# Kernel tuning notes

Hardware: AMD Instinct MI355X
Metric: run time of the kernel (lower is better)

The kernel has to match this reference:

```python
import jax, jax.numpy as jnp
import numpy as np

RADIUS = 1.0
NSAMPLE = 8
GROUPS = 8
EPS = 1e-5


def setup_inputs() -> dict:
    key = jax.random.key(0)
    ks = jax.random.split(key, 8)
    b, n_p, dim, C = 4, 4096, 128, 64
    coords = jax.random.normal(ks[0], (b, n_p, 3), jnp.float32)
    xyz2 = jax.random.normal(ks[1], (b, n_p, 3), jnp.float32)
    fmap1 = jax.random.normal(ks[2], (b, dim, n_p), jnp.float32)
    fmap2 = jax.random.normal(ks[3], (b, dim, n_p), jnp.float32)
    conv_w = jax.random.normal(ks[4], (C, 4), jnp.float32) * 0.1
    conv_b = jnp.zeros((C,), jnp.float32)
    gn_gamma = jnp.ones((C,), jnp.float32)
    gn_beta = jnp.zeros((C,), jnp.float32)
    prelu_a = jnp.full((1,), 0.25, jnp.float32)
    out_w = jax.random.normal(ks[5], (C, C), jnp.float32) * 0.1
    out_b = jnp.zeros((C,), jnp.float32)
    return {"coords": coords, "xyz2": xyz2, "fmap1": fmap1, "fmap2": fmap2,
            "conv_w": conv_w, "conv_b": conv_b, "gn_gamma": gn_gamma,
            "gn_beta": gn_beta, "prelu_a": prelu_a, "out_w": out_w, "out_b": out_b}


def ball_query(xyz2, coords, radius, nsample):
    # first-nsample points of xyz2 within `radius` of each query in coords,
    # padded with the first valid index (0 if none) -- matches PointNet++ ball query.
    n = xyz2.shape[1]
    d2 = jnp.sum((coords[:, :, None, :] - xyz2[:, None, :, :]) ** 2, axis=-1)  # [b,m,n]
    j = jnp.arange(n, dtype=jnp.float32)
    score = jnp.where(d2 < radius * radius, -j, -float(n))  # larger score = earlier valid idx
    vals, _ = jax.lax.top_k(score, nsample)  # [b,m,nsample]
    valid = vals > -float(n)
    idx = (-vals).astype(jnp.int32)
    first = jnp.where(valid[..., :1], idx[..., :1], 0)
    return jnp.where(valid, idx, first)  # [b,m,nsample]


def reference(coords, xyz2, fmap1, fmap2, conv_w, conv_b, gn_gamma, gn_beta, prelu_a, out_w, out_b):
    b, n_p, _ = coords.shape
    dim = fmap1.shape[1]
    # corr = fmap1^T fmap2 / sqrt(dim): [b, n_p, n_p]
    corr = jnp.einsum('bdn,bdm->bnm', fmap1, fmap2) / jnp.sqrt(jnp.float32(dim))
    idx = ball_query(xyz2, coords, RADIUS, NSAMPLE)  # [b,n_p,nsample]
    # grouped_xyz: xyz2[idx] - coords -> [b, 3, n_p, nsample]
    gathered = jax.vmap(lambda pts, ind: pts[ind])(xyz2, idx)  # [b,n_p,ns,3]
    grouped_xyz = jnp.transpose(gathered - coords[:, :, None, :], (0, 3, 1, 2))
    # corr gather along source dim
    cur_corr = jnp.take_along_axis(corr, idx, axis=2)[:, None]  # [b,1,n_p,ns]
    feat = jnp.concatenate([cur_corr, grouped_xyz], axis=1)  # [b,4,n_p,ns]
    # 1x1 Conv2d
    x = jnp.einsum('oc,bcns->bons', conv_w, feat) + conv_b[None, :, None, None]
    # GroupNorm(8, 64)
    C = x.shape[1]
    xg = x.reshape(b, GROUPS, C // GROUPS, n_p, NSAMPLE)
    mu = jnp.mean(xg, axis=(2, 3, 4), keepdims=True)
    var = jnp.var(xg, axis=(2, 3, 4), keepdims=True)
    xg = (xg - mu) * jax.lax.rsqrt(var + EPS)
    x = xg.reshape(b, C, n_p, NSAMPLE) * gn_gamma[None, :, None, None] + gn_beta[None, :, None, None]
    # PReLU (single shared slope)
    x = jnp.where(x >= 0, x, prelu_a[0] * x)
    # max over neighbors
    x = jnp.max(x, axis=3)  # [b,64,n_p]
    # 1x1 Conv1d out
    return jnp.einsum('oc,bcn->bon', out_w, x) + out_b[None, :, None]
```

## Files before the change

### kernel.cpp

```cpp
#include <hip/hip_runtime.h>
#include <hip/hip_cooperative_groups.h>
#include <math.h>

namespace cg = cooperative_groups;

#define B 4
#define NP 4096
#define DIM 128
#define CCH 64
#define NS 8

struct TrS { float tile[128][31]; };
struct K2S { float As[16 * 132]; float red[4][14]; };
struct K3S {
  float4 vs4[256]; float4 ow4[1024];
  float cw[256], cb[64], Av[64], Bv[64], ob[64];
  float red2[8][14], Sm[14], SxA[64], SxxA[64];
};
struct SM {
  float4 fs4[128];
  int sidx[128];
  union { TrS tr; K2S k2; K3S k3; } u;
};

__global__ __launch_bounds__(256, 4) void fused_all(
    const float* __restrict__ coords, const float* __restrict__ xyz2,
    const float* __restrict__ f1, const float* __restrict__ f2,
    const float* __restrict__ conv_w, const float* __restrict__ conv_b,
    const float* __restrict__ gamma, const float* __restrict__ beta,
    const float* __restrict__ prelu, const float* __restrict__ out_w,
    const float* __restrict__ out_b, float* __restrict__ out,
    float* __restrict__ f2T, float* __restrict__ parts, int useT) {
  cg::grid_group grid = cg::this_grid();
  __shared__ SM sm;
  int blk = blockIdx.x;
  int t = threadIdx.x;
  int bq = (blk & 7) >> 1;
  int chunk = ((blk >> 3) << 1) | (blk & 1);
  int m0 = chunk * 16;

  if (useT) {
    int b = blk >> 8;
    int n0 = (blk & 255) * 16;
    const float* s = f2 + (size_t)b * DIM * NP;
    float* dd = f2T + (size_t)b * NP * DIM;
#pragma unroll
    for (int it = 0; it < 2; ++it) {
      int f = t + it * 256;
      int d = f >> 2, ng = f & 3;
      float4 v = *(const float4*)&s[(size_t)d * NP + n0 + ng * 4];
      int aw = 5 * (d >> 5);
      sm.u.tr.tile[d][ng * 4 + 0 + aw] = v.x;
      sm.u.tr.tile[d][ng * 4 + 1 + aw] = v.y;
      sm.u.tr.tile[d][ng * 4 + 2 + aw] = v.z;
      sm.u.tr.tile[d][ng * 4 + 3 + aw] = v.w;
    }
    __syncthreads();
#pragma unroll
    for (int it = 0; it < 2; ++it) {
      int f = t + it * 256;
      int n = f >> 5, dg = f & 31;
      int ar = 5 * (dg >> 3);
      float4 w;
      w.x = sm.u.tr.tile[dg * 4 + 0][n + ar];
      w.y = sm.u.tr.tile[dg * 4 + 1][n + ar];
      w.z = sm.u.tr.tile[dg * 4 + 2][n + ar];
      w.w = sm.u.tr.tile[dg * 4 + 3][n + ar];
      *(float4*)&dd[(size_t)(n0 + n) * DIM + dg * 4] = w;
    }
  }

  {
    int wv = t >> 6, lane = t & 63;
    const float* xz = xyz2 + (size_t)bq * NP * 3;
#pragma unroll 1
    for (int qi = 0; qi < 4; ++qi) {
      int m = m0 + wv * 4 + qi;
      const float* cp = coords + ((size_t)bq * NP + m) * 3;
      float cx = cp[0], cy = cp[1], cz = cp[2];
      int j0 = lane * 3;
      float px = xz[j0], py = xz[j0 + 1], pz = xz[j0 + 2];
      int cnt = 0, first = 0;
      bool any = false;
      for (int c = 0; c < 64 && cnt < NS; ++c) {
        int cn = (c < 63) ? c + 1 : 63;
        int jn = (cn * 64 + lane) * 3;
        float nx = xz[jn], ny = xz[jn + 1], nz = xz[jn + 2];
        float dx = __fsub_rn(cx, px);
        float dy = __fsub_rn(cy, py);
        float dz = __fsub_rn(cz, pz);
        float d2 = __fadd_rn(__fadd_rn(__fmul_rn(dx, dx), __fmul_rn(dy, dy)),
                             __fmul_rn(dz, dz));
        bool hit = d2 < 1.0f;
        unsigned long long mk = __ballot(hit);
        if (mk) {
          int rank = cnt + __popcll(mk & ((1ull << lane) - 1ull));
          if (hit && rank < NS) sm.sidx[(wv * 4 + qi) * NS + rank] = c * 64 + lane;
          if (!any) {
            first = c * 64 + (__ffsll((long long)mk) - 1);
            any = true;
          }
          cnt += __popcll(mk);
        }
        px = nx; py = ny; pz = nz;
      }
      if (lane < NS && lane >= cnt)
        sm.sidx[(wv * 4 + qi) * NS + lane] = first;
    }
  }

  grid.sync();

  {
    K2S& k2 = sm.u.k2;
    int b = bq;
    if (useT) {
#pragma unroll
      for (int pass = 0; pass < 2; ++pass) {
        int d = pass * 64 + (t >> 2);
        int j4 = t & 3;
        float4 v = *(const float4*)&f1[(size_t)(b * DIM + d) * NP + m0 + j4 * 4];
        k2.As[(j4 * 4 + 0) * 132 + d] = v.x;
        k2.As[(j4 * 4 + 1) * 132 + d] = v.y;
        k2.As[(j4 * 4 + 2) * 132 + d] = v.z;
        k2.As[(j4 * 4 + 3) * 132 + d] = v.w;
      }
    }
    __syncthreads();

    int g = t >> 3;
    int l = t & 7;
    int idv[4];
#pragma unroll
    for (int r = 0; r < 4; ++r) idv[r] = sm.sidx[r * 32 + g];

    float pm[14];
#pragma unroll
    for (int k = 0; k < 14; ++k) pm[k] = 0.f;

#pragma unroll
    for (int r = 0; r < 4; ++r) {
      int pi = r * 32 + g;
      int m = pi >> 3;
      int id = idv[r];
      float acc = 0.f;
      if (useT) {
        const float4* brow = (const float4*)(f2T + ((size_t)b * NP + id) * DIM);
        const float4* arow = (const float4*)&k2.As[m * 132];
#pragma unroll
        for (int k = 0; k < 4; ++k) {
          float4 y = brow[l + 8 * k];
          float4 x = arow[l + 8 * k];
          acc += x.x * y.x + x.y * y.y + x.z * y.z + x.w * y.w;
        }
      } else {
#pragma unroll
        for (int k = 0; k < 4; ++k) {
#pragma unroll
          for (int c = 0; c < 4; ++c) {
            int d = (l + 8 * k) * 4 + c;
            acc += f1[(size_t)(b * DIM + d) * NP + m0 + m] *
                   f2[(size_t)(b * DIM + d) * NP + id];
          }
        }
      }
      acc += __shfl_xor(acc, 1);
      acc += __shfl_xor(acc, 2);
      acc += __shfl_xor(acc, 4);
      float corr = acc * 0.08838834764831843f;
      const float* cp = coords + ((size_t)b * NP + m0 + m) * 3;
      const float* xp = xyz2 + ((size_t)b * NP + id) * 3;
      float dx = xp[0] - cp[0], dy = xp[1] - cp[1], dz = xp[2] - cp[2];
      if (l == 0) {
        float4 fv;
        fv.x = corr; fv.y = dx; fv.z = dy; fv.w = dz;
        sm.fs4[pi] = fv;
      }
      pm[0] += corr; pm[1] += dx; pm[2] += dy; pm[3] += dz;
      pm[4] += corr * corr; pm[5] += corr * dx; pm[6] += corr * dy;
      pm[7] += corr * dz; pm[8] += dx * dx; pm[9] += dx * dy;
      pm[10] += dx * dz; pm[11] += dy * dy; pm[12] += dy * dz; pm[13] += dz * dz;
    }
#pragma unroll
    for (int k = 0; k < 14; ++k) {
      float v = pm[k];
#pragma unroll
      for (int off = 32; off; off >>= 1) v += __shfl_xor(v, off);
      pm[k] = v;
    }
    int lane = t & 63, wvv = t >> 6;
    if (lane == 0) {
#pragma unroll
      for (int k = 0; k < 14; ++k) k2.red[wvv][k] = pm[k];
    }
    __syncthreads();
    if (t < 14) {
      float ssum = (k2.red[0][t] + k2.red[1][t] + k2.red[2][t] + k2.red[3][t]) * 0.125f;
      parts[((size_t)bq * 256 + chunk) * 14 + t] = ssum;
    }
  }

  grid.sync();

  {
    K3S& kb = sm.u.k3;
    int b = bq;
    int n0 = m0;
    {
      const float4* src = (const float4*)out_w;
#pragma unroll
      for (int k = 0; k < 4; ++k) {
        int i4 = t + k * 256;
        int oo = i4 >> 4, gg = i4 & 15;
        kb.ow4[oo * 16 + (gg ^ ((oo >> 2) & 7))] = src[i4];
      }
    }
    kb.cw[t] = conv_w[t];
    if (t < 64) {
      kb.cb[t] = conv_b[t];
      kb.ob[t] = out_b[t];
    }
    if (t < 112) {
      int k = t % 14, jg = t / 14;
      float s = 0.f;
      const float* pp = parts + ((size_t)b * 256 + jg * 32) * 14 + k;
      for (int j = 0; j < 32; ++j) s += pp[j * 14];
      kb.red2[jg][k] = s;
    }
    float alpha = prelu[0];
    __syncthreads();
    if (t < 14) {
      float s = 0.f;
#pragma unroll
      for (int jg = 0; jg < 8; ++jg) s += kb.red2[jg][t];
      kb.Sm[t] = s;
    }
    __syncthreads();
    if (t < 64) {
      int o = t;
      float w0 = kb.cw[o * 4 + 0], w1 = kb.cw[o * 4 + 1];
      float w2 = kb.cw[o * 4 + 2], w3 = kb.cw[o * 4 + 3];
      float bo = kb.cb[o];
      const float cnt = (float)(NP * NS);
      float wS1 = w0 * kb.Sm[0] + w1 * kb.Sm[1] + w2 * kb.Sm[2] + w3 * kb.Sm[3];
      float q = w0 * w0 * kb.Sm[4] + w1 * w1 * kb.Sm[8] + w2 * w2 * kb.Sm[11] +
                w3 * w3 * kb.Sm[13] +
                2.f * (w0 * w1 * kb.Sm[5] + w0 * w2 * kb.Sm[6] + w0 * w3 * kb.Sm[7] +
                       w1 * w2 * kb.Sm[9] + w1 * w3 * kb.Sm[10] + w2 * w3 * kb.Sm[12]);
      kb.SxA[o] = wS1 + bo * cnt;
      kb.SxxA[o] = q + 2.f * bo * wS1 + bo * bo * cnt;
    }
    __syncthreads();
    if (t < 64) {
      int o = t, g = o >> 3;
      const float cnt = (float)(NP * NS);
      float sm_ = 0.f, s2 = 0.f;
#pragma unroll
      for (int k = 0; k < 8; ++k) {
        sm_ += kb.SxA[g * 8 + k];
        s2 += kb.SxxA[g * 8 + k];
      }
      float mean = sm_ / (cnt * 8.f);
      float e2 = s2 / (cnt * 8.f);
      float var = e2 - mean * mean;
      float inv = rsqrtf(var + 1e-5f);
      float A = gamma[o] * inv;
      kb.Av[o] = A;
      kb.Bv[o] = beta[o] - mean * A;
    }
    __syncthreads();

    {
      int o = t & 63;
      int pw = t >> 6;
      float w0 = kb.cw[o * 4 + 0], w1 = kb.cw[o * 4 + 1];
      float w2 = kb.cw[o * 4 + 2], w3 = kb.cw[o * 4 + 3];
      float A = kb.Av[o], Bc = kb.Bv[o], bb = kb.cb[o];
      float* vsf = (float*)kb.vs4;
#pragma unroll
      for (int i = 0; i < 4; ++i) {
        int p = pw * 4 + i;
        float mx = -INFINITY;
#pragma unroll
        for (int s = 0; s < NS; ++s) {
          float4 f = sm.fs4[p * 8 + s];
          float x = fmaf(w0, f.x, fmaf(w1, f.y, fmaf(w2, f.z, fmaf(w3, f.w, bb))));
          float y = fmaf(A, x, Bc);
          y = (y >= 0.f) ? y : alpha * y;
          mx = fmaxf(mx, y);
        }
        vsf[(p * 16 + ((o >> 2) ^ ((p >> 2) & 7))) * 4 + (o & 3)] = mx;
      }
    }
    __syncthreads();

    {
      int ti = t >> 3;
      int tj = t & 7;
      float acc[2][2];
#pragma unroll
      for (int oi = 0; oi < 2; ++oi)
#pragma unroll
        for (int pj = 0; pj < 2; ++pj) acc[oi][pj] = 0.f;
#pragma unroll
      for (int g = 0; g < 16; ++g) {
        float4 vv[2], ww[2];
#pragma unroll
        for (int pj = 0; pj < 2; ++pj) {
          int p = tj * 2 + pj;
          vv[pj] = kb.vs4[p * 16 + (g ^ ((p >> 2) & 7))];
        }
#pragma unroll
        for (int oi = 0; oi < 2; ++oi) {
          int oo = ti * 2 + oi;
          ww[oi] = kb.ow4[oo * 16 + (g ^ ((oo >> 2) & 7))];
        }
#pragma unroll
        for (int oi = 0; oi < 2; ++oi)
#pragma unroll
          for (int pj = 0; pj < 2; ++pj) {
            acc[oi][pj] = fmaf(ww[oi].x, vv[pj].x, acc[oi][pj]);
            acc[oi][pj] = fmaf(ww[oi].y, vv[pj].y, acc[oi][pj]);
            acc[oi][pj] = fmaf(ww[oi].z, vv[pj].z, acc[oi][pj]);
            acc[oi][pj] = fmaf(ww[oi].w, vv[pj].w, acc[oi][pj]);
          }
      }
#pragma unroll
      for (int oi = 0; oi < 2; ++oi) {
        int oo = ti * 2 + oi;
        float bb = kb.ob[oo];
        float2 r;
        r.x = acc[oi][0] + bb;
        r.y = acc[oi][1] + bb;
        *(float2*)&out[((size_t)b * CCH + oo) * NP + n0 + tj * 2] = r;
      }
    }
  }
}

__global__ __launch_bounds__(256) void kA_bq_transpose(
    const float* __restrict__ coords, const float* __restrict__ xyz2,
    int* __restrict__ idxb, const float* __restrict__ f2,
    float* __restrict__ o2) {
  int blk = blockIdx.x;
  int t = threadIdx.x;
  __shared__ float tile[128][33];
  if (blk < B * NP) {
    int b = blk >> 12, m = blk & (NP - 1);
    int wv = t >> 6, lane = t & 63;
    const float* cp = coords + ((size_t)b * NP + m) * 3;
    float cx = cp[0], cy = cp[1], cz = cp[2];
    const float* xz = xyz2 + (size_t)b * NP * 3;
    int base = wv * 1024;
    int j0 = (base + lane) * 3;
    float px = xz[j0], py = xz[j0 + 1], pz = xz[j0 + 2];
    int cnt = 0, myidx = 0;
    for (int c = 0; c < 16 && cnt < NS; ++c) {
      int cn = (c < 15) ? c + 1 : 15;
      int jn = (base + cn * 64 + lane) * 3;
      float nx = xz[jn], ny = xz[jn + 1], nz = xz[jn + 2];
      float dx = __fsub_rn(cx, px);
      float dy = __fsub_rn(cy, py);
      float dz = __fsub_rn(cz, pz);
      float d2 = __fadd_rn(__fadd_rn(__fmul_rn(dx, dx), __fmul_rn(dy, dy)),
                           __fmul_rn(dz, dz));
      unsigned long long mk = __ballot(d2 < 1.0f);
      while (mk && cnt < NS) {
        int bpos = __ffsll(mk) - 1;
        int jf = base + c * 64 + bpos;
        if (lane == cnt) myidx = jf;
        ++cnt;
        mk &= mk - 1;
      }
      px = nx; py = ny; pz = nz;
    }
    __shared__ int sidx[4][NS];
    __shared__ int scnt[4];
    if (lane < NS) sidx[wv][lane] = myidx;
    if (lane == 0) scnt[wv] = cnt;
    __syncthreads();
    if (t < NS) {
      int c0 = scnt[0], c1 = scnt[1], c2 = scnt[2], c3 = scnt[3];
      int total = c0 + c1 + c2 + c3;
      int v;
      if (t < c0) v = sidx[0][t];
      else if (t < c0 + c1) v = sidx[1][t - c0];
      else if (t < c0 + c1 + c2) v = sidx[2][t - c0 - c1];
      else if (t < total) v = sidx[3][t - c0 - c1 - c2];
      else v = (c0 > 0) ? sidx[0][0]
             : (c1 > 0) ? sidx[1][0]
             : (c2 > 0) ? sidx[2][0]
             : (c3 > 0) ? sidx[3][0] : 0;
      idxb[((size_t)b * NP + m) * NS + t] = v;
    }
  } else {
    int tb = blk - B * NP;
    int b = tb >> 7;
    int n0 = (tb & 127) * 32;
    const float* s = f2 + (size_t)b * DIM * NP;
    float* d = o2 + (size_t)b * NP * DIM;
    int dr = t >> 3;
    int ng = t & 7;
#pragma unroll
    for (int k = 0; k < 4; ++k) {
      int dd = dr + 32 * k;
      float4 v = *(const float4*)&s[(size_t)dd * NP + n0 + ng * 4];
      tile[dd][ng * 4 + 0] = v.x;
      tile[dd][ng * 4 + 1] = v.y;
      tile[dd][ng * 4 + 2] = v.z;
      tile[dd][ng * 4 + 3] = v.w;
    }
    __syncthreads();
    int n = t >> 3;
#pragma unroll
    for (int k = 0; k < 4; ++k) {
      int d0 = (t & 7) * 4 + 32 * k;
      float4 w;
      w.x = tile[d0 + 0][n];
      w.y = tile[d0 + 1][n];
      w.z = tile[d0 + 2][n];
      w.w = tile[d0 + 3][n];
      *(float4*)&d[(size_t)(n0 + n) * DIM + d0] = w;
    }
  }
}

__global__ __launch_bounds__(256) void k2_corrfeat(
    const float* __restrict__ f1, const float* __restrict__ f2T,
    const float* __restrict__ coords, const float* __restrict__ xyz2,
    const int* __restrict__ idxb, float* __restrict__ feat,
    float* __restrict__ parts, int trans) {
  int i = blockIdx.x;
  int b = (i & 7) >> 1;
  int chunk = ((i >> 3) << 1) | (i & 1);
  int m0 = chunk * 16;
  int t = threadIdx.x;
  __shared__ float As[16 * 132];
  __shared__ float red[4][14];
  if (trans) {
#pragma unroll
    for (int pass = 0; pass < 2; ++pass) {
      int d = pass * 64 + (t >> 2);
      int j4 = t & 3;
      float4 v = *(const float4*)&f1[(size_t)(b * DIM + d) * NP + m0 + j4 * 4];
      As[(j4 * 4 + 0) * 132 + d] = v.x;
      As[(j4 * 4 + 1) * 132 + d] = v.y;
      As[(j4 * 4 + 2) * 132 + d] = v.z;
      As[(j4 * 4 + 3) * 132 + d] = v.w;
    }
  }
  __syncthreads();
  int g = t >> 3;
  int l = t & 7;
  size_t ibase = ((size_t)b * NP + m0) * NS;
  int idv[4];
#pragma unroll
  for (int r = 0; r < 4; ++r) idv[r] = idxb[ibase + r * 32 + g];
  float pm[14];
#pragma unroll
  for (int k = 0; k < 14; ++k) pm[k] = 0.f;
#pragma unroll
  for (int r = 0; r < 4; ++r) {
    int pi = r * 32 + g;
    int m = pi >> 3, s = pi & 7;
    int id = idv[r];
    float acc = 0.f;
    if (trans) {
      const float4* brow = (const float4*)(f2T + ((size_t)b * NP + id) * DIM);
      const float4* arow = (const float4*)&As[m * 132];
#pragma unroll
      for (int k = 0; k < 4; ++k) {
        float4 y = brow[l + 8 * k];
        float4 x = arow[l + 8 * k];
        acc += x.x * y.x + x.y * y.y + x.z * y.z + x.w * y.w;
      }
    } else {
#pragma unroll
      for (int k = 0; k < 4; ++k) {
#pragma unroll
        for (int c = 0; c < 4; ++c) {
          int d = (l + 8 * k) * 4 + c;
          acc += f1[(size_t)(b * DIM + d) * NP + m0 + m] *
                 f2T[(size_t)(b * DIM + d) * NP + id];
        }
      }
    }
    acc += __shfl_xor(acc, 1);
    acc += __shfl_xor(acc, 2);
    acc += __shfl_xor(acc, 4);
    float corr = acc * 0.08838834764831843f;
    const float* cp = coords + ((size_t)b * NP + m0 + m) * 3;
    const float* xp = xyz2 + ((size_t)b * NP + id) * 3;
    float dx = xp[0] - cp[0], dy = xp[1] - cp[1], dz = xp[2] - cp[2];
    if (l == 0) {
      float4 fv;
      fv.x = corr; fv.y = dx; fv.z = dy; fv.w = dz;
      ((float4*)feat)[((size_t)b * NP + m0 + m) * NS + s] = fv;
    }
    pm[0] += corr; pm[1] += dx; pm[2] += dy; pm[3] += dz;
    pm[4] += corr * corr; pm[5] += corr * dx; pm[6] += corr * dy;
    pm[7] += corr * dz; pm[8] += dx * dx; pm[9] += dx * dy;
    pm[10] += dx * dz; pm[11] += dy * dy; pm[12] += dy * dz; pm[13] += dz * dz;
  }
#pragma unroll
  for (int k = 0; k < 14; ++k) {
    float v = pm[k];
#pragma unroll
    for (int off = 32; off; off >>= 1) v += __shfl_xor(v, off);
    pm[k] = v;
  }
  int lane = t & 63, wvv = t >> 6;
  if (lane == 0) {
#pragma unroll
    for (int k = 0; k < 14; ++k) red[wvv][k] = pm[k];
  }
  __syncthreads();
  if (t < 14) {
    float ssum = (red[0][t] + red[1][t] + red[2][t] + red[3][t]) * 0.125f;
    parts[((size_t)b * 256 + chunk) * 14 + t] = ssum;
  }
}

__global__ __launch_bounds__(256) void kB_out(
    const float* __restrict__ feat, const float* __restrict__ parts,
    const float* __restrict__ conv_w, const float* __restrict__ conv_b,
    const float* __restrict__ gamma, const float* __restrict__ beta,
    const float* __restrict__ prelu, const float* __restrict__ out_w,
    const float* __restrict__ out_b, float* __restrict__ out) {
  int b = blockIdx.x >> 8;
  int n0 = (blockIdx.x & 255) * 16;
  __shared__ float4 fs4[16 * 8];
  __shared__ float4 vs4[16 * 16];
  __shared__ float4 ow4[64 * 16];
  __shared__ float cw[256], cb_[64], Av[64], Bv[64], ob_[64];
  __shared__ float red2[8][14];
  __shared__ float Sm[14];
  __shared__ float SxA[64], SxxA[64];
  int t = threadIdx.x;
  if (t < 128) fs4[t] = ((const float4*)(feat + ((size_t)b * NP + n0) * 32))[t];
  {
    const float4* src = (const float4*)out_w;
#pragma unroll
    for (int k = 0; k < 4; ++k) {
      int i4 = t + k * 256;
      int oo = i4 >> 4, gg = i4 & 15;
      ow4[oo * 16 + (gg ^ ((oo >> 2) & 7))] = src[i4];
    }
  }
  cw[t] = conv_w[t];
  if (t < 64) {
    cb_[t] = conv_b[t];
    ob_[t] = out_b[t];
  }
  if (t < 112) {
    int k = t % 14, jg = t / 14;
    float s = 0.f;
    const float* pp = parts + ((size_t)b * 256 + jg * 32) * 14 + k;
    for (int j = 0; j < 32; ++j) s += pp[j * 14];
    red2[jg][k] = s;
  }
  float alpha = prelu[0];
  __syncthreads();
  if (t < 14) {
    float s = 0.f;
#pragma unroll
    for (int jg = 0; jg < 8; ++jg) s += red2[jg][t];
    Sm[t] = s;
  }
  __syncthreads();
  if (t < 64) {
    int o = t;
    float w0 = cw[o * 4 + 0], w1 = cw[o * 4 + 1];
    float w2 = cw[o * 4 + 2], w3 = cw[o * 4 + 3];
    float bo = cb_[o];
    const float cnt = (float)(NP * NS);
    float wS1 = w0 * Sm[0] + w1 * Sm[1] + w2 * Sm[2] + w3 * Sm[3];
    float q = w0 * w0 * Sm[4] + w1 * w1 * Sm[8] + w2 * w2 * Sm[11] +
              w3 * w3 * Sm[13] +
              2.f * (w0 * w1 * Sm[5] + w0 * w2 * Sm[6] + w0 * w3 * Sm[7] +
                     w1 * w2 * Sm[9] + w1 * w3 * Sm[10] + w2 * w3 * Sm[12]);
    SxA[o] = wS1 + bo * cnt;
    SxxA[o] = q + 2.f * bo * wS1 + bo * bo * cnt;
  }
  __syncthreads();
  if (t < 64) {
    int o = t, g = o >> 3;
    const float cnt = (float)(NP * NS);
    float sm = 0.f, s2 = 0.f;
#pragma unroll
    for (int k = 0; k < 8; ++k) {
      sm += SxA[g * 8 + k];
      s2 += SxxA[g * 8 + k];
    }
    float mean = sm / (cnt * 8.f);
    float e2 = s2 / (cnt * 8.f);
    float var = e2 - mean * mean;
    float inv = rsqrtf(var + 1e-5f);
    float A = gamma[o] * inv;
    Av[o] = A;
    Bv[o] = beta[o] - mean * A;
  }
  __syncthreads();
  {
    int o = t & 63;
    int pw = t >> 6;
    float w0 = cw[o * 4 + 0], w1 = cw[o * 4 + 1];
    float w2 = cw[o * 4 + 2], w3 = cw[o * 4 + 3];
    float A = Av[o], Bc = Bv[o], bb = cb_[o];
    float* vsf = (float*)vs4;
#pragma unroll
    for (int i = 0; i < 4; ++i) {
      int p = pw * 4 + i;
      float mx = -INFINITY;
#pragma unroll
      for (int s = 0; s < NS; ++s) {
        float4 f = fs4[p * 8 + s];
        float x = fmaf(w0, f.x, fmaf(w1, f.y, fmaf(w2, f.z, fmaf(w3, f.w, bb))));
        float y = fmaf(A, x, Bc);
        y = (y >= 0.f) ? y : alpha * y;
        mx = fmaxf(mx, y);
      }
      vsf[(p * 16 + ((o >> 2) ^ ((p >> 2) & 7))) * 4 + (o & 3)] = mx;
    }
  }
  __syncthreads();
  {
    int ti = t >> 3;
    int tj = t & 7;
    float acc[2][2];
#pragma unroll
    for (int oi = 0; oi < 2; ++oi)
#pragma unroll
      for (int pj = 0; pj < 2; ++pj) acc[oi][pj] = 0.f;
#pragma unroll
    for (int g = 0; g < 16; ++g) {
      float4 vv[2], ww[2];
#pragma unroll
      for (int pj = 0; pj < 2; ++pj) {
        int p = tj * 2 + pj;
        vv[pj] = vs4[p * 16 + (g ^ ((p >> 2) & 7))];
      }
#pragma unroll
      for (int oi = 0; oi < 2; ++oi) {
        int oo = ti * 2 + oi;
        ww[oi] = ow4[oo * 16 + (g ^ ((oo >> 2) & 7))];
      }
#pragma unroll
      for (int oi = 0; oi < 2; ++oi)
#pragma unroll
        for (int pj = 0; pj < 2; ++pj) {
          acc[oi][pj] = fmaf(ww[oi].x, vv[pj].x, acc[oi][pj]);
          acc[oi][pj] = fmaf(ww[oi].y, vv[pj].y, acc[oi][pj]);
          acc[oi][pj] = fmaf(ww[oi].z, vv[pj].z, acc[oi][pj]);
          acc[oi][pj] = fmaf(ww[oi].w, vv[pj].w, acc[oi][pj]);
        }
    }
#pragma unroll
    for (int oi = 0; oi < 2; ++oi) {
      int oo = ti * 2 + oi;
      float bb = ob_[oo];
      float2 r;
      r.x = acc[oi][0] + bb;
      r.y = acc[oi][1] + bb;
      *(float2*)&out[((size_t)b * CCH + oo) * NP + n0 + tj * 2] = r;
    }
  }
}

extern "C" void kernel_launch(void* const* d_in, const int* in_sizes, int n_in,
                              void* d_out, int out_size, void* d_ws, size_t ws_size,
                              hipStream_t stream) {
  const float* coords = (const float*)d_in[0];
  const float* xyz2 = (const float*)d_in[1];
  const float* fmap1 = (const float*)d_in[2];
  const float* fmap2 = (const float*)d_in[3];
  const float* conv_w = (const float*)d_in[4];
  const float* conv_b = (const float*)d_in[5];
  const float* gamma = (const float*)d_in[6];
  const float* beta = (const float*)d_in[7];
  const float* prelu = (const float*)d_in[8];
  const float* out_w = (const float*)d_in[9];
  const float* out_b = (const float*)d_in[10];
  float* out = (float*)d_out;
  float* ws = (float*)d_ws;

  const size_t BND = (size_t)B * NP * DIM;
  const size_t FEAT = (size_t)B * NP * NS * 4;
  const size_t PARTS = (size_t)B * 256 * 14;
  size_t needT = (BND + FEAT + PARTS + 512) * sizeof(float) +
                 (size_t)B * NP * NS * sizeof(int);
  int useT = (ws_size >= needT) ? 1 : 0;

  float* f2T = ws;
  float* featp = useT ? (f2T + BND) : ws;
  float* parts = featp + FEAT;
  int* idxp = (int*)(parts + PARTS + 512);

  int maxBlocks = 0;
  hipError_t oe = hipOccupancyMaxActiveBlocksPerMultiprocessor(
      &maxBlocks, fused_all, 256, 0);
  if (oe == hipSuccess && maxBlocks >= 4) {
    void* args[] = {(void*)&coords, (void*)&xyz2,   (void*)&fmap1,
                    (void*)&fmap2,  (void*)&conv_w, (void*)&conv_b,
                    (void*)&gamma,  (void*)&beta,   (void*)&prelu,
                    (void*)&out_w,  (void*)&out_b,  (void*)&out,
                    (void*)&f2T,    (void*)&parts,  (void*)&useT};
    hipError_t le = hipLaunchCooperativeKernel(
        fused_all, dim3(1024), dim3(256), args, 0, stream);
    if (le == hipSuccess) return;
  }

  int nblk = B * NP + (useT ? (B * (NP / 32)) : 0);
  kA_bq_transpose<<<dim3(nblk), dim3(256), 0, stream>>>(coords, xyz2, idxp,
                                                        fmap2, f2T);
  k2_corrfeat<<<dim3(1024), dim3(256), 0, stream>>>(
      fmap1, useT ? f2T : fmap2, coords, xyz2, idxp, featp, parts, useT);
  kB_out<<<dim3(B * (NP / 16)), dim3(256), 0, stream>>>(
      featp, parts, conv_w, conv_b, gamma, beta, prelu, out_w, out_b, out);
}
```

Before: 50.22 us.

## Interleave ball-query queries, prefetch gathered rows, and hoist weight loads before grid syncs

The ball query now handles all four queries of a wave together in one pass over xyz2 chunks, two chunks per iteration, and exits early once every query has found its neighbours. This shares the point loads across queries and exposes more independent work. The corr phase issues the gathered f2T and xyz2 loads before staging f1 into shared memory, so that latency overlaps the shared-memory fill. Output and conv weights are loaded into shared memory before the first grid sync so that cost moves off the final phase, and the transpose tile now uses float4 stores with a new padding. In exchange, shared memory grows because the weights are no longer in the union, which may reduce occupancy or the cooperative grid capacity.

```diff
diff --git a/kernel.cpp b/kernel.cpp
--- a/kernel.cpp
+++ b/kernel.cpp
@@ -10,17 +10,20 @@
 #define CCH 64
 #define NS 8
 
-struct TrS { float tile[128][31]; };
-struct K2S { float As[16 * 132]; float red[4][14]; };
-struct K3S {
-  float4 vs4[256]; float4 ow4[1024];
-  float cw[256], cb[64], Av[64], Bv[64], ob[64];
-  float red2[8][14], Sm[14], SxA[64], SxxA[64];
-};
 struct SM {
   float4 fs4[128];
   int sidx[128];
-  union { TrS tr; K2S k2; K3S k3; } u;
+  float4 ow4[1024];
+  float cw[256];
+  float cb[64], ob[64];
+  union {
+    float tile[128][35];
+    struct { float As[16 * 132]; float red[4][14]; } k2;
+    struct {
+      float4 vs4[256];
+      float Av[64], Bv[64], red2[8][14], Sm[14], SxA[64], SxxA[64];
+    } k3;
+  } u;
 };
 
 __global__ __launch_bounds__(256, 4) void fused_all(
@@ -49,23 +52,19 @@
       int f = t + it * 256;
       int d = f >> 2, ng = f & 3;
       float4 v = *(const float4*)&s[(size_t)d * NP + n0 + ng * 4];
-      int aw = 5 * (d >> 5);
-      sm.u.tr.tile[d][ng * 4 + 0 + aw] = v.x;
-      sm.u.tr.tile[d][ng * 4 + 1 + aw] = v.y;
-      sm.u.tr.tile[d][ng * 4 + 2 + aw] = v.z;
-      sm.u.tr.tile[d][ng * 4 + 3 + aw] = v.w;
+      *(float4*)&sm.u.tile[d][ng * 4 + (d >> 5)] = v;
     }
     __syncthreads();
 #pragma unroll
     for (int it = 0; it < 2; ++it) {
       int f = t + it * 256;
       int n = f >> 5, dg = f & 31;
-      int ar = 5 * (dg >> 3);
+      int ar = dg >> 3;
       float4 w;
-      w.x = sm.u.tr.tile[dg * 4 + 0][n + ar];
-      w.y = sm.u.tr.tile[dg * 4 + 1][n + ar];
-      w.z = sm.u.tr.tile[dg * 4 + 2][n + ar];
-      w.w = sm.u.tr.tile[dg * 4 + 3][n + ar];
+      w.x = sm.u.tile[dg * 4 + 0][n + ar];
+      w.y = sm.u.tile[dg * 4 + 1][n + ar];
+      w.z = sm.u.tile[dg * 4 + 2][n + ar];
+      w.w = sm.u.tile[dg * 4 + 3][n + ar];
       *(float4*)&dd[(size_t)(n0 + n) * DIM + dg * 4] = w;
     }
   }
@@ -73,48 +72,117 @@
   {
     int wv = t >> 6, lane = t & 63;
     const float* xz = xyz2 + (size_t)bq * NP * 3;
+    float cx[4], cy[4], cz[4];
+#pragma unroll
+    for (int qi = 0; qi < 4; ++qi) {
+      const float* cp = coords + ((size_t)bq * NP + m0 + wv * 4 + qi) * 3;
+      cx[qi] = cp[0]; cy[qi] = cp[1]; cz[qi] = cp[2];
+    }
+    int cnt[4] = {0, 0, 0, 0};
+    int first[4] = {0, 0, 0, 0};
+    int j0 = lane * 3;
+    float ax = xz[j0], ay = xz[j0 + 1], az = xz[j0 + 2];
+    int j1 = (64 + lane) * 3;
+    float bx = xz[j1], by = xz[j1 + 1], bz = xz[j1 + 2];
 #pragma unroll 1
+    for (int c = 0; c < 64; c += 2) {
+      int c2 = (c + 2 < 64) ? c + 2 : 63;
+      int c3 = (c + 3 < 64) ? c + 3 : 63;
+      int jn2 = (c2 * 64 + lane) * 3, jn3 = (c3 * 64 + lane) * 3;
+      float nax = xz[jn2], nay = xz[jn2 + 1], naz = xz[jn2 + 2];
+      float nbx = xz[jn3], nby = xz[jn3 + 1], nbz = xz[jn3 + 2];
+#pragma unroll
+      for (int qi = 0; qi < 4; ++qi) {
+        if (cnt[qi] < NS) {
+          float dx = __fsub_rn(cx[qi], ax);
+          float dy = __fsub_rn(cy[qi], ay);
+          float dz = __fsub_rn(cz[qi], az);
+          float d2 = __fadd_rn(__fadd_rn(__fmul_rn(dx, dx), __fmul_rn(dy, dy)),
+                               __fmul_rn(dz, dz));
+          bool hit = d2 < 1.0f;
+          unsigned long long mk = __ballot(hit);
+          if (mk) {
+            int rank = cnt[qi] + __popcll(mk & ((1ull << lane) - 1ull));
+            if (hit && rank < NS)
+              sm.sidx[(wv * 4 + qi) * NS + rank] = c * 64 + lane;
+            if (cnt[qi] == 0) first[qi] = c * 64 + (__ffsll(mk) - 1);
+            cnt[qi] += __popcll(mk);
+          }
+        }
+      }
+      if ((cnt[0] >= NS) & (cnt[1] >= NS) & (cnt[2] >= NS) & (cnt[3] >= NS))
+        break;
+#pragma unroll
+      for (int qi = 0; qi < 4; ++qi) {
+        if (cnt[qi] < NS) {
+          float dx = __fsub_rn(cx[qi], bx);
+          float dy = __fsub_rn(cy[qi], by);
+          float dz = __fsub_rn(cz[qi], bz);
+          float d2 = __fadd_rn(__fadd_rn(__fmul_rn(dx, dx), __fmul_rn(dy, dy)),
+                               __fmul_rn(dz, dz));
+          bool hit = d2 < 1.0f;
+          unsigned long long mk = __ballot(hit);
+          if (mk) {
+            int rank = cnt[qi] + __popcll(mk & ((1ull << lane) - 1ull));
+            if (hit && rank < NS)
+              sm.sidx[(wv * 4 + qi) * NS + rank] = (c + 1) * 64 + lane;
+            if (cnt[qi] == 0) first[qi] = (c + 1) * 64 + (__ffsll(mk) - 1);
+            cnt[qi] += __popcll(mk);
+          }
+        }
+      }
+      if ((cnt[0] >= NS) & (cnt[1] >= NS) & (cnt[2] >= NS) & (cnt[3] >= NS))
+        break;
+      ax = nax; ay = nay; az = naz;
+      bx = nbx; by = nby; bz = nbz;
+    }
+#pragma unroll
     for (int qi = 0; qi < 4; ++qi) {
-      int m = m0 + wv * 4 + qi;
-      const float* cp = coords + ((size_t)bq * NP + m) * 3;
-      float cx = cp[0], cy = cp[1], cz = cp[2];
-      int j0 = lane * 3;
-      float px = xz[j0], py = xz[j0 + 1], pz = xz[j0 + 2];
-      int cnt = 0, first = 0;
-      bool any = false;
-      for (int c = 0; c < 64 && cnt < NS; ++c) {
-        int cn = (c < 63) ? c + 1 : 63;
-        int jn = (cn * 64 + lane) * 3;
-        float nx = xz[jn], ny = xz[jn + 1], nz = xz[jn + 2];
-        float dx = __fsub_rn(cx, px);
-        float dy = __fsub_rn(cy, py);
-        float dz = __fsub_rn(cz, pz);
-        float d2 = __fadd_rn(__fadd_rn(__fmul_rn(dx, dx), __fmul_rn(dy, dy)),
-                             __fmul_rn(dz, dz));
-        bool hit = d2 < 1.0f;
-        unsigned long long mk = __ballot(hit);
-        if (mk) {
-          int rank = cnt + __popcll(mk & ((1ull << lane) - 1ull));
-          if (hit && rank < NS) sm.sidx[(wv * 4 + qi) * NS + rank] = c * 64 + lane;
-          if (!any) {
-            first = c * 64 + (__ffsll((long long)mk) - 1);
-            any = true;
-          }
-          cnt += __popcll(mk);
-        }
-        px = nx; py = ny; pz = nz;
-      }
-      if (lane < NS && lane >= cnt)
-        sm.sidx[(wv * 4 + qi) * NS + lane] = first;
+      if (lane < NS && lane >= cnt[qi])
+        sm.sidx[(wv * 4 + qi) * NS + lane] = first[qi];
+    }
+  }
+
+  {
+    const float4* src = (const float4*)out_w;
+#pragma unroll
+    for (int k = 0; k < 4; ++k) {
+      int i4 = t + k * 256;
+      int oo = i4 >> 4, gg = i4 & 15;
+      sm.ow4[oo * 16 + (gg ^ ((oo >> 2) & 7))] = src[i4];
+    }
+    sm.cw[t] = conv_w[t];
+    if (t < 64) {
+      sm.cb[t] = conv_b[t];
+      sm.ob[t] = out_b[t];
     }
   }
 
   grid.sync();
 
   {
-    K2S& k2 = sm.u.k2;
+    auto& k2 = sm.u.k2;
     int b = bq;
+    int g = t >> 3;
+    int l = t & 7;
+    float pm[14];
+#pragma unroll
+    for (int k = 0; k < 14; ++k) pm[k] = 0.f;
+
     if (useT) {
+      int id0 = sm.sidx[g], id1 = sm.sidx[32 + g];
+      int id2 = sm.sidx[64 + g], id3 = sm.sidx[96 + g];
+      const float4* br0 = (const float4*)(f2T + ((size_t)b * NP + id0) * DIM) + l;
+      const float4* br1 = (const float4*)(f2T + ((size_t)b * NP + id1) * DIM) + l;
+      const float4* br2 = (const float4*)(f2T + ((size_t)b * NP + id2) * DIM) + l;
+      const float4* br3 = (const float4*)(f2T + ((size_t)b * NP + id3) * DIM) + l;
+      float4 y00 = br0[0], y01 = br0[8], y02 = br0[16], y03 = br0[24];
+      float4 y10 = br1[0], y11 = br1[8], y12 = br1[16], y13 = br1[24];
+      const float* xq0 = xyz2 + ((size_t)b * NP + id0) * 3;
+      const float* xq1 = xyz2 + ((size_t)b * NP + id1) * 3;
+      float x0x = xq0[0], x0y = xq0[1], x0z = xq0[2];
+      float x1x = xq1[0], x1y = xq1[1], x1z = xq1[2];
+
 #pragma unroll
       for (int pass = 0; pass < 2; ++pass) {
         int d = pass * 64 + (t >> 2);
@@ -125,35 +193,57 @@
         k2.As[(j4 * 4 + 2) * 132 + d] = v.z;
         k2.As[(j4 * 4 + 3) * 132 + d] = v.w;
       }
-    }
-    __syncthreads();
-
-    int g = t >> 3;
-    int l = t & 7;
-    int idv[4];
-#pragma unroll
-    for (int r = 0; r < 4; ++r) idv[r] = sm.sidx[r * 32 + g];
-
-    float pm[14];
-#pragma unroll
-    for (int k = 0; k < 14; ++k) pm[k] = 0.f;
-
-#pragma unroll
-    for (int r = 0; r < 4; ++r) {
-      int pi = r * 32 + g;
-      int m = pi >> 3;
-      int id = idv[r];
-      float acc = 0.f;
-      if (useT) {
-        const float4* brow = (const float4*)(f2T + ((size_t)b * NP + id) * DIM);
-        const float4* arow = (const float4*)&k2.As[m * 132];
-#pragma unroll
-        for (int k = 0; k < 4; ++k) {
-          float4 y = brow[l + 8 * k];
-          float4 x = arow[l + 8 * k];
-          acc += x.x * y.x + x.y * y.y + x.z * y.z + x.w * y.w;
-        }
-      } else {
+      __syncthreads();
+      float4 y20 = br2[0], y21 = br2[8], y22 = br2[16], y23 = br2[24];
+      float4 y30 = br3[0], y31 = br3[8], y32 = br3[16], y33 = br3[24];
+      const float* xq2 = xyz2 + ((size_t)b * NP + id2) * 3;
+      const float* xq3 = xyz2 + ((size_t)b * NP + id3) * 3;
+      float x2x = xq2[0], x2y = xq2[1], x2z = xq2[2];
+      float x3x = xq3[0], x3y = xq3[1], x3z = xq3[2];
+
+#define DO_R(r, ya, yb, yc, yd, nxx, nxy, nxz)                                 \
+      {                                                                        \
+        int pi = (r) * 32 + g;                                                 \
+        int m = pi >> 3;                                                       \
+        const float4* arow = (const float4*)&k2.As[m * 132] + l;               \
+        float4 a0 = arow[0], a1 = arow[8], a2 = arow[16], a3 = arow[24];       \
+        float acc = a0.x * ya.x + a0.y * ya.y + a0.z * ya.z + a0.w * ya.w +    \
+                    a1.x * yb.x + a1.y * yb.y + a1.z * yb.z + a1.w * yb.w +    \
+                    a2.x * yc.x + a2.y * yc.y + a2.z * yc.z + a2.w * yc.w +    \
+                    a3.x * yd.x + a3.y * yd.y + a3.z * yd.z + a3.w * yd.w;     \
+        acc += __shfl_xor(acc, 1);                                             \
+        acc += __shfl_xor(acc, 2);                                             \
+        acc += __shfl_xor(acc, 4);                                             \
+        float corr = acc * 0.08838834764831843f;                               \
+        const float* cpq = coords + ((size_t)b * NP + m0 + m) * 3;             \
+        float dx = nxx - cpq[0], dy = nxy - cpq[1], dz = nxz - cpq[2];         \
+        if (l == 0) {                                                          \
+          float4 fv;                                                           \
+          fv.x = corr; fv.y = dx; fv.z = dy; fv.w = dz;                        \
+          sm.fs4[pi] = fv;                                                     \
+        }                                                                      \
+        pm[0] += corr; pm[1] += dx; pm[2] += dy; pm[3] += dz;                  \
+        pm[4] += corr * corr; pm[5] += corr * dx; pm[6] += corr * dy;          \
+        pm[7] += corr * dz; pm[8] += dx * dx; pm[9] += dx * dy;                \
+        pm[10] += dx * dz; pm[11] += dy * dy; pm[12] += dy * dz;               \
+        pm[13] += dz * dz;                                                     \
+      }
+      DO_R(0, y00, y01, y02, y03, x0x, x0y, x0z)
+      DO_R(1, y10, y11, y12, y13, x1x, x1y, x1z)
+      DO_R(2, y20, y21, y22, y23, x2x, x2y, x2z)
+      DO_R(3, y30, y31, y32, y33, x3x, x3y, x3z)
+#undef DO_R
+    } else {
+      __syncthreads();
+      int idv[4];
+#pragma unroll
+      for (int r = 0; r < 4; ++r) idv[r] = sm.sidx[r * 32 + g];
+#pragma unroll
+      for (int r = 0; r < 4; ++r) {
+        int pi = r * 32 + g;
+        int m = pi >> 3;
+        int id = idv[r];
+        float acc = 0.f;
 #pragma unroll
         for (int k = 0; k < 4; ++k) {
 #pragma unroll
@@ -163,24 +253,26 @@
                    f2[(size_t)(b * DIM + d) * NP + id];
           }
         }
-      }
-      acc += __shfl_xor(acc, 1);
-      acc += __shfl_xor(acc, 2);
-      acc += __shfl_xor(acc, 4);
-      float corr = acc * 0.08838834764831843f;
-      const float* cp = coords + ((size_t)b * NP + m0 + m) * 3;
-      const float* xp = xyz2 + ((size_t)b * NP + id) * 3;
-      float dx = xp[0] - cp[0], dy = xp[1] - cp[1], dz = xp[2] - cp[2];
-      if (l == 0) {
-        float4 fv;
-        fv.x = corr; fv.y = dx; fv.z = dy; fv.w = dz;
-        sm.fs4[pi] = fv;
-      }
-      pm[0] += corr; pm[1] += dx; pm[2] += dy; pm[3] += dz;
-      pm[4] += corr * corr; pm[5] += corr * dx; pm[6] += corr * dy;
-      pm[7] += corr * dz; pm[8] += dx * dx; pm[9] += dx * dy;
-      pm[10] += dx * dz; pm[11] += dy * dy; pm[12] += dy * dz; pm[13] += dz * dz;
-    }
+        acc += __shfl_xor(acc, 1);
+        acc += __shfl_xor(acc, 2);
+        acc += __shfl_xor(acc, 4);
+        float corr = acc * 0.08838834764831843f;
+        const float* cpq = coords + ((size_t)b * NP + m0 + m) * 3;
+        const float* xp = xyz2 + ((size_t)b * NP + id) * 3;
+        float dx = xp[0] - cpq[0], dy = xp[1] - cpq[1], dz = xp[2] - cpq[2];
+        if (l == 0) {
+          float4 fv;
+          fv.x = corr; fv.y = dx; fv.z = dy; fv.w = dz;
+          sm.fs4[pi] = fv;
+        }
+        pm[0] += corr; pm[1] += dx; pm[2] += dy; pm[3] += dz;
+        pm[4] += corr * corr; pm[5] += corr * dx; pm[6] += corr * dy;
+        pm[7] += corr * dz; pm[8] += dx * dx; pm[9] += dx * dy;
+        pm[10] += dx * dz; pm[11] += dy * dy; pm[12] += dy * dz;
+        pm[13] += dz * dz;
+      }
+    }
+
 #pragma unroll
     for (int k = 0; k < 14; ++k) {
       float v = pm[k];
@@ -203,27 +295,14 @@
   grid.sync();
 
   {
-    K3S& kb = sm.u.k3;
+    auto& kb = sm.u.k3;
     int b = bq;
     int n0 = m0;
-    {
-      const float4* src = (const float4*)out_w;
-#pragma unroll
-      for (int k = 0; k < 4; ++k) {
-        int i4 = t + k * 256;
-        int oo = i4 >> 4, gg = i4 & 15;
-        kb.ow4[oo * 16 + (gg ^ ((oo >> 2) & 7))] = src[i4];
-      }
-    }
-    kb.cw[t] = conv_w[t];
-    if (t < 64) {
-      kb.cb[t] = conv_b[t];
-      kb.ob[t] = out_b[t];
-    }
     if (t < 112) {
       int k = t % 14, jg = t / 14;
       float s = 0.f;
       const float* pp = parts + ((size_t)b * 256 + jg * 32) * 14 + k;
+#pragma unroll 8
       for (int j = 0; j < 32; ++j) s += pp[j * 14];
       kb.red2[jg][k] = s;
     }
@@ -238,9 +317,9 @@
     __syncthreads();
     if (t < 64) {
       int o = t;
-      float w0 = kb.cw[o * 4 + 0], w1 = kb.cw[o * 4 + 1];
-      float w2 = kb.cw[o * 4 + 2], w3 = kb.cw[o * 4 + 3];
-      float bo = kb.cb[o];
+      float w0 = sm.cw[o * 4 + 0], w1 = sm.cw[o * 4 + 1];
+      float w2 = sm.cw[o * 4 + 2], w3 = sm.cw[o * 4 + 3];
+      float bo = sm.cb[o];
       const float cnt = (float)(NP * NS);
       float wS1 = w0 * kb.Sm[0] + w1 * kb.Sm[1] + w2 * kb.Sm[2] + w3 * kb.Sm[3];
       float q = w0 * w0 * kb.Sm[4] + w1 * w1 * kb.Sm[8] + w2 * w2 * kb.Sm[11] +
@@ -273,9 +352,9 @@
     {
       int o = t & 63;
       int pw = t >> 6;
-      float w0 = kb.cw[o * 4 + 0], w1 = kb.cw[o * 4 + 1];
-      float w2 = kb.cw[o * 4 + 2], w3 = kb.cw[o * 4 + 3];
-      float A = kb.Av[o], Bc = kb.Bv[o], bb = kb.cb[o];
+      float w0 = sm.cw[o * 4 + 0], w1 = sm.cw[o * 4 + 1];
+      float w2 = sm.cw[o * 4 + 2], w3 = sm.cw[o * 4 + 3];
+      float A = kb.Av[o], Bc = kb.Bv[o], bb = sm.cb[o];
       float* vsf = (float*)kb.vs4;
 #pragma unroll
       for (int i = 0; i < 4; ++i) {
@@ -313,7 +392,7 @@
 #pragma unroll
         for (int oi = 0; oi < 2; ++oi) {
           int oo = ti * 2 + oi;
-          ww[oi] = kb.ow4[oo * 16 + (g ^ ((oo >> 2) & 7))];
+          ww[oi] = sm.ow4[oo * 16 + (g ^ ((oo >> 2) & 7))];
         }
 #pragma unroll
         for (int oi = 0; oi < 2; ++oi)
@@ -328,7 +407,7 @@
 #pragma unroll
       for (int oi = 0; oi < 2; ++oi) {
         int oo = ti * 2 + oi;
-        float bb = kb.ob[oo];
+        float bb = sm.ob[oo];
         float2 r;
         r.x = acc[oi][0] + bb;
         r.y = acc[oi][1] + bb;
```

After: 50.35 us. About the same (+0.3%).
